# Performance work log

Measured on AMD Instinct MI355X. Metric: run time of the kernel, lower is better.

Reference implementation:

```python
import jax, jax.numpy as jnp
import numpy as np
from jax import lax

DIM = 512
HEADS = 8
HEAD_DIM = DIM // HEADS
FS = 56            # features_size -> H = W = 56
SR = 2             # sr_ratio
N = FS * FS        # query tokens = 3136
KN = (FS // SR) ** 2  # kv tokens = 784
B = 4
SCALE = HEAD_DIM ** -0.5
LN_EPS = 1e-5


def _relative_indices(fs):
    # matches generate_relative_distance: [[x, y] for x in range(fs) for y in range(fs)]
    coords = np.stack(np.meshgrid(np.arange(fs), np.arange(fs), indexing='ij'), -1).reshape(-1, 2)
    dist = coords[None, :, :] - coords[:, None, :] + (fs - 1)   # (N, N, 2), values in [0, 2fs-2]
    return jnp.asarray(dist, dtype=jnp.int32)


def setup_inputs() -> dict:
    key = jax.random.key(0)
    ks = jax.random.split(key, 8)
    s = 0.02
    return {
        'x':    jax.random.normal(ks[0], (B, DIM, FS, FS), jnp.float32),
        'Wq':   jax.random.normal(ks[1], (DIM, DIM), jnp.float32) * s,
        'Wkv':  jax.random.normal(ks[2], (DIM, 2 * DIM), jnp.float32) * s,
        'Wsr':  jax.random.normal(ks[3], (DIM, DIM, SR, SR), jnp.float32) * s,  # OIHW
        'b_sr': jnp.zeros((DIM,), jnp.float32),
        'gamma': jnp.ones((DIM,), jnp.float32),
        'beta':  jnp.zeros((DIM,), jnp.float32),
        'Wp':   jax.random.normal(ks[4], (DIM, DIM), jnp.float32) * s,
        'bp':   jnp.zeros((DIM,), jnp.float32),
        'pos':  jax.random.normal(ks[5], (2 * FS - 1, 2 * FS - 1), jnp.float32) * 0.2,
        'rel_idx': _relative_indices(FS),
    }


def reference(x, Wq, Wkv, Wsr, b_sr, gamma, beta, Wp, bp, pos, rel_idx):
    b, c, h, w = x.shape
    n = h * w
    xq = x.reshape(b, c, n).transpose(0, 2, 1)                      # B N C
    q = (xq @ Wq).reshape(b, n, HEADS, HEAD_DIM).transpose(0, 2, 1, 3)  # B h N d

    # spatial reduction of k/v: Conv2d(k=SR, s=SR) + LayerNorm
    xr = lax.conv_general_dilated(x, Wsr, (SR, SR), 'VALID',
                                  dimension_numbers=('NCHW', 'OIHW', 'NCHW'))
    xr = xr + b_sr[None, :, None, None]
    kn = xr.shape[2] * xr.shape[3]
    xkv = xr.reshape(b, c, kn).transpose(0, 2, 1)                   # B KN C
    mu = xkv.mean(-1, keepdims=True)
    var = ((xkv - mu) ** 2).mean(-1, keepdims=True)
    xkv = (xkv - mu) * lax.rsqrt(var + LN_EPS) * gamma + beta

    # kv projection; rearrange 'B N (dim h l) -> l B h N dim'
    kv = (xkv @ Wkv).reshape(b, kn, HEAD_DIM, HEADS, 2)
    k = kv[..., 0].transpose(0, 3, 1, 2)                            # B h KN d
    v = kv[..., 1].transpose(0, 3, 1, 2)                            # B h KN d

    attn = jnp.einsum('bhnd,bhmd->bhnm', q, k) * SCALE              # B h N KN
    bias = pos[rel_idx[:, :kn, 0], rel_idx[:, :kn, 1]]              # N KN gathered bias
    attn = jax.nn.softmax(attn + bias, axis=-1)

    out = jnp.einsum('bhnm,bhmd->bhnd', attn, v)                    # B h N d
    out = out.transpose(0, 2, 1, 3).reshape(b, n, c)                # B N C
    out = out @ Wp + bp
    return out.transpose(0, 2, 1).reshape(b, c, h, w)
```

## Files before the change

kernel.cpp:

```cpp
#include <hip/hip_runtime.h>
#include <hip/hip_bf16.h>
#include <cstdint>

constexpr int BATCH = 4;
constexpr int CDIM  = 512;
constexpr int NHEAD = 8;
constexpr int HD    = 64;
constexpr int FSP   = 56;
constexpr int NTOK  = FSP * FSP;
constexpr int KH    = 28;
constexpr int KNTOK = KH * KH;
constexpr float SCALE_ATT = 0.125f;
constexpr int BIAS_LD = 832;

typedef _Float16 f16;
typedef __attribute__((ext_vector_type(8))) _Float16 half8;
typedef __attribute__((ext_vector_type(4))) float  floatx4;

__global__ __launch_bounds__(256) void k_tsplit(const float* __restrict__ in,
                                                f16* __restrict__ oh,
                                                int R, int C,
                                                size_t inb, size_t outb) {
  __shared__ float t[64][65];
  const int tid = threadIdx.x;
  in += (size_t)blockIdx.z * inb;
  oh += (size_t)blockIdx.z * outb;
  const int r0 = blockIdx.x * 64, c0 = blockIdx.y * 64;
  const int rr = tid >> 2, cs = (tid & 3) * 16;
  const float* src = in + (size_t)(r0 + rr) * C + c0 + cs;
#pragma unroll
  for (int j = 0; j < 16; j += 4) *(float4*)&t[rr][cs + j] = *(const float4*)&src[j];
  __syncthreads();
  f16* dh = oh + (size_t)(c0 + rr) * R + r0 + cs;
#pragma unroll
  for (int j = 0; j < 16; ++j) dh[j] = (f16)t[cs + j][rr];
}

__global__ __launch_bounds__(256) void k_srprep(const float* __restrict__ Wsr,
                                                f16* __restrict__ oh) {
  const int o = blockIdx.x;
  const float* src = Wsr + (size_t)o * 2048;
  f16* dh = oh + (size_t)o * 2048;
  for (int kp = threadIdx.x; kp < 2048; kp += 256) {
    const int dd = kp >> 9, c = kp & 511;
    dh[kp] = (f16)src[c * 4 + dd];
  }
}

#define GSTR 40
struct GemmSmem { f16 A[128][GSTR]; f16 B[128][GSTR]; };

__device__ __forceinline__ void gemm_loop(GemmSmem* sm,
                                          const f16* __restrict__ aP,
                                          const f16* __restrict__ bP,
                                          int sr, int ss, int wm, int wn,
                                          int quad, int tx,
                                          floatx4 acc[4][4]) {
  half8 ra0 = *(const half8*)&aP[0];
  half8 ra1 = *(const half8*)&aP[8];
  half8 rb0 = *(const half8*)&bP[0];
  half8 rb1 = *(const half8*)&bP[8];
  for (int it = 0; it < 16; ++it) {
    *(half8*)&sm->A[sr][ss]     = ra0;
    *(half8*)&sm->A[sr][ss + 8] = ra1;
    *(half8*)&sm->B[sr][ss]     = rb0;
    *(half8*)&sm->B[sr][ss + 8] = rb1;
    __syncthreads();
    if (it + 1 < 16) {
      const f16* an = aP + (it + 1) * 32;
      const f16* bn = bP + (it + 1) * 32;
      ra0 = *(const half8*)&an[0]; ra1 = *(const half8*)&an[8];
      rb0 = *(const half8*)&bn[0]; rb1 = *(const half8*)&bn[8];
    }
    half8 ah[4];
#pragma unroll
    for (int i = 0; i < 4; ++i)
      ah[i] = *(const half8*)&sm->A[wm * 64 + i * 16 + tx][quad * 8];
#pragma unroll
    for (int j = 0; j < 4; ++j) {
      const half8 bh = *(const half8*)&sm->B[wn * 64 + j * 16 + tx][quad * 8];
#pragma unroll
      for (int i = 0; i < 4; ++i)
        acc[i][j] = __builtin_amdgcn_mfma_f32_16x16x32_f16(ah[i], bh, acc[i][j], 0, 0, 0);
    }
    __syncthreads();
  }
}

#define GEMM_PRE()                                                        \
  const int tid = threadIdx.x, lane = tid & 63, wv = tid >> 6;            \
  const int wm = wv & 1, wn = wv >> 1, quad = lane >> 4, tx = lane & 15;  \
  const int sr = tid >> 1, ss = (tid & 1) * 16;                           \
  floatx4 acc[4][4];                                                      \
  _Pragma("unroll") for (int i = 0; i < 4; ++i)                           \
  _Pragma("unroll") for (int j = 0; j < 4; ++j)                           \
      acc[i][j] = (floatx4){0.f, 0.f, 0.f, 0.f};

__global__ __launch_bounds__(256) void k_srconv(const f16* __restrict__ xT,
                                                const f16* __restrict__ WsrP,
                                                float* __restrict__ XRp) {
  __shared__ GemmSmem sm;
  const int m0 = blockIdx.x * 128, n0 = blockIdx.y * 128;
  const int b = blockIdx.z >> 2, kc = blockIdx.z & 3;
  GEMM_PRE();
  int am = m0 + sr; if (am >= KNTOK) am = 0;
  const int ii = am / KH, jj = am % KH;
  const int sp = 112 * ii + 2 * jj + (kc >> 1) * FSP + (kc & 1);
  const f16* aP = xT + (size_t)b * NTOK * CDIM + (size_t)sp * CDIM + ss;
  const f16* bP = WsrP + (size_t)(n0 + sr) * 2048 + kc * 512 + ss;
  gemm_loop(&sm, aP, bP, sr, ss, wm, wn, quad, tx, acc);
  float* dst = XRp + (size_t)(kc * BATCH + b) * KNTOK * CDIM;
#pragma unroll
  for (int i = 0; i < 4; ++i)
#pragma unroll
    for (int rg = 0; rg < 4; ++rg) {
      const int m = m0 + wm * 64 + i * 16 + quad * 4 + rg;
      if (m >= KNTOK) continue;
#pragma unroll
      for (int j = 0; j < 4; ++j)
        dst[(size_t)m * CDIM + n0 + wn * 64 + j * 16 + tx] = acc[i][j][rg];
    }
}

__global__ __launch_bounds__(256) void k_ln(const float* __restrict__ XRp,
                                            const float* __restrict__ b_sr,
                                            const float* __restrict__ gamma,
                                            const float* __restrict__ beta,
                                            f16* __restrict__ oh) {
  const int row = blockIdx.x;
  const size_t slab = (size_t)BATCH * KNTOK * CDIM;
  const float* p = XRp + (size_t)row * CDIM;
  const int tid = threadIdx.x;
  const float v0 = p[tid] + p[tid + slab] + p[tid + 2 * slab] + p[tid + 3 * slab]
                 + b_sr[tid];
  const float v1 = p[tid + 256] + p[tid + 256 + slab] + p[tid + 256 + 2 * slab]
                 + p[tid + 256 + 3 * slab] + b_sr[tid + 256];
  float s = v0 + v1;
  float s2 = v0 * v0 + v1 * v1;
#pragma unroll
  for (int mask = 32; mask >= 1; mask >>= 1) {
    s  += __shfl_xor(s, mask, 64);
    s2 += __shfl_xor(s2, mask, 64);
  }
  __shared__ float ws[4], ws2[4];
  const int wid = tid >> 6;
  if ((tid & 63) == 0) { ws[wid] = s; ws2[wid] = s2; }
  __syncthreads();
  const float ts  = ws[0] + ws[1] + ws[2] + ws[3];
  const float ts2 = ws2[0] + ws2[1] + ws2[2] + ws2[3];
  const float mu  = ts * (1.f / CDIM);
  const float var = ts2 * (1.f / CDIM) - mu * mu;
  const float rs  = rsqrtf(var + 1e-5f);
  const size_t base = (size_t)row * CDIM;
  oh[base + tid]       = (f16)((v0 - mu) * rs * gamma[tid] + beta[tid]);
  oh[base + tid + 256] = (f16)((v1 - mu) * rs * gamma[tid + 256] + beta[tid + 256]);
}

__global__ __launch_bounds__(256) void k_qkv(const f16* __restrict__ xT,
                                             const f16* __restrict__ WqT,
                                             f16* __restrict__ Qh,
                                             const f16* __restrict__ XRh,
                                             const f16* __restrict__ WkvT,
                                             f16* __restrict__ Kh,
                                             f16* __restrict__ Vt) {
  __shared__ GemmSmem sm;
  GEMM_PRE();
  int bid = blockIdx.x;
  if (bid < 400) {
    const int b = bid / 100, t = bid % 100;
    const int m0 = (t >> 2) * 128, n0 = (t & 3) * 128;
    int arow = m0 + sr; if (arow >= NTOK) arow = NTOK - 1;
    const f16* aP = xT + (size_t)b * NTOK * CDIM + (size_t)arow * CDIM + ss;
    const f16* bP = WqT + (size_t)(n0 + sr) * CDIM + ss;
    gemm_loop(&sm, aP, bP, sr, ss, wm, wn, quad, tx, acc);
    f16* qhB = Qh + (size_t)b * NTOK * CDIM;
#pragma unroll
    for (int i = 0; i < 4; ++i)
#pragma unroll
      for (int rg = 0; rg < 4; ++rg) {
        const int m = m0 + wm * 64 + i * 16 + quad * 4 + rg;
        if (m >= NTOK) continue;
#pragma unroll
        for (int j = 0; j < 4; ++j)
          qhB[(size_t)m * CDIM + n0 + wn * 64 + j * 16 + tx] = (f16)acc[i][j][rg];
      }
  } else {
    bid -= 400;
    const int b = bid / 56, w = bid % 56, nt = w / 7, mt = w % 7;
    const int m0 = mt * 128, n0 = nt * 128;
    int arow = m0 + sr; if (arow >= KNTOK) arow = KNTOK - 1;
    const f16* aP = XRh + (size_t)b * KNTOK * CDIM + (size_t)arow * CDIM + ss;
    const f16* bP = WkvT + (size_t)(n0 + sr) * CDIM + ss;
    gemm_loop(&sm, aP, bP, sr, ss, wm, wn, quad, tx, acc);
#pragma unroll
    for (int i = 0; i < 4; ++i)
#pragma unroll
      for (int rg = 0; rg < 4; ++rg) {
        const int m = m0 + wm * 64 + i * 16 + quad * 4 + rg;
        if (m >= KNTOK) continue;
#pragma unroll
        for (int j = 0; j < 4; ++j) {
          const int o2 = n0 + wn * 64 + j * 16 + tx;
          const int d = o2 >> 4, hh = (o2 >> 1) & 7;
          const float v = acc[i][j][rg];
          if (o2 & 1)
            Vt[((size_t)(b * NHEAD + hh) * HD + d) * KNTOK + m] = (f16)v;
          else
            Kh[((size_t)(b * NHEAD + hh) * KNTOK + m) * HD + d] = (f16)v;
        }
      }
  }
}

__global__ __launch_bounds__(256) void k_bias(const int* __restrict__ rel,
                                              const float* __restrict__ pos,
                                              float* __restrict__ biasT) {
  const int n = blockIdx.x;
  for (int i = threadIdx.x; i < BIAS_LD; i += 256) {
    const int jc = i >> 6, w = i & 63, txx = w >> 2, tt = w & 3;
    const int m = jc * 64 + tt * 16 + txx;
    float v = -30000.f;
    if (m < KNTOK) {
      const size_t o = ((size_t)n * NTOK + m) * 2;
      v = pos[rel[o] * 111 + rel[o + 1]];
    }
    biasT[(size_t)n * BIAS_LD + i] = v;
  }
}

#define LSTR 72
__global__ __launch_bounds__(256) void k_attn(const f16* __restrict__ Qh,
                                              const f16* __restrict__ Kh,
                                              const f16* __restrict__ Vt,
                                              const float* __restrict__ biasT,
                                              f16* __restrict__ Oh) {
  __shared__ f16 Qhs[64][LSTR], Khs[64][LSTR], Vts[64][LSTR];
  __shared__ f16 Ps[4][16][LSTR];
  const int b = blockIdx.x >> 3, h = blockIdx.x & 7;
  const int n0 = blockIdx.y * 64;
  const int tid = threadIdx.x, lane = tid & 63, wv = tid >> 6;
  const int quad = lane >> 4, tx = lane & 15;
  const int rr = tid >> 2, sg = (tid & 3) * 16;

  const f16* qhB = Qh + ((size_t)b * NTOK + n0) * CDIM + h * HD;
  const f16* khB = Kh + (size_t)(b * NHEAD + h) * KNTOK * HD;
  const f16* vtB = Vt + (size_t)(b * NHEAD + h) * HD * KNTOK;

  {
    const size_t off = (size_t)rr * CDIM + sg;
    *(half8*)&Qhs[rr][sg]     = *(const half8*)&qhB[off];
    *(half8*)&Qhs[rr][sg + 8] = *(const half8*)&qhB[off + 8];
  }

  size_t bbase_r[4];
#pragma unroll
  for (int r = 0; r < 4; ++r) {
    const int grow = n0 + wv * 16 + quad * 4 + r;
    bbase_r[r] = (size_t)grow * BIAS_LD + tx * 4;
  }

  floatx4 acc_o[4];
#pragma unroll
  for (int t = 0; t < 4; ++t) acc_o[t] = (floatx4){0.f, 0.f, 0.f, 0.f};
  float l_part[4] = {0.f, 0.f, 0.f, 0.f};
  __syncthreads();

  for (int jc = 0; jc < 13; ++jc) {
    const int mb = jc * 64;
    const half8 z = {0, 0, 0, 0, 0, 0, 0, 0};
    {
      const int m = mb + rr;
      if (m < KNTOK) {
        const size_t off = (size_t)m * HD + sg;
        *(half8*)&Khs[rr][sg]     = *(const half8*)&khB[off];
        *(half8*)&Khs[rr][sg + 8] = *(const half8*)&khB[off + 8];
      } else {
        *(half8*)&Khs[rr][sg] = z; *(half8*)&Khs[rr][sg + 8] = z;
      }
      if (mb + sg < KNTOK) {
        const size_t voff = (size_t)rr * KNTOK + mb + sg;
        *(half8*)&Vts[rr][sg]     = *(const half8*)&vtB[voff];
        *(half8*)&Vts[rr][sg + 8] = *(const half8*)&vtB[voff + 8];
      } else {
        *(half8*)&Vts[rr][sg] = z; *(half8*)&Vts[rr][sg + 8] = z;
      }
    }
    __syncthreads();

    floatx4 sc[4];
#pragma unroll
    for (int t = 0; t < 4; ++t) sc[t] = (floatx4){0.f, 0.f, 0.f, 0.f};
#pragma unroll
    for (int ks = 0; ks < 2; ++ks) {
      const int kk = ks * 32 + quad * 8;
      const half8 aqh = *(const half8*)&Qhs[wv * 16 + tx][kk];
#pragma unroll
      for (int t = 0; t < 4; ++t) {
        const half8 bkh = *(const half8*)&Khs[t * 16 + tx][kk];
        sc[t] = __builtin_amdgcn_mfma_f32_16x16x32_f16(aqh, bkh, sc[t], 0, 0, 0);
      }
    }

#pragma unroll
    for (int r = 0; r < 4; ++r) {
      const float4 bb = *(const float4*)&biasT[bbase_r[r] + jc * 64];
      const float p0 = __expf(fmaf(sc[0][r], SCALE_ATT, bb.x));
      const float p1 = __expf(fmaf(sc[1][r], SCALE_ATT, bb.y));
      const float p2 = __expf(fmaf(sc[2][r], SCALE_ATT, bb.z));
      const float p3 = __expf(fmaf(sc[3][r], SCALE_ATT, bb.w));
      l_part[r] += (p0 + p1) + (p2 + p3);
      const int prow = quad * 4 + r;
      Ps[wv][prow][0 * 16 + tx] = (f16)p0;
      Ps[wv][prow][1 * 16 + tx] = (f16)p1;
      Ps[wv][prow][2 * 16 + tx] = (f16)p2;
      Ps[wv][prow][3 * 16 + tx] = (f16)p3;
    }

#pragma unroll
    for (int ks = 0; ks < 2; ++ks) {
      const int kk = ks * 32 + quad * 8;
      const half8 ap = *(const half8*)&Ps[wv][tx][kk];
#pragma unroll
      for (int t = 0; t < 4; ++t) {
        const half8 bv = *(const half8*)&Vts[t * 16 + tx][kk];
        acc_o[t] = __builtin_amdgcn_mfma_f32_16x16x32_f16(ap, bv, acc_o[t], 0, 0, 0);
      }
    }
    __syncthreads();
  }

#pragma unroll
  for (int r = 0; r < 4; ++r) {
    float l = l_part[r];
#pragma unroll
    for (int msk = 1; msk < 16; msk <<= 1) l += __shfl_xor(l, msk, 64);
    const float inv = 1.f / l;
    const int grow = n0 + wv * 16 + quad * 4 + r;
    const size_t base = ((size_t)b * NTOK + grow) * CDIM + h * HD;
#pragma unroll
    for (int t = 0; t < 4; ++t)
      Oh[base + t * 16 + tx] = (f16)(acc_o[t][r] * inv);
  }
}

__global__ __launch_bounds__(256) void k_outproj(const f16* __restrict__ ah_,
                                                 const f16* __restrict__ wh,
                                                 const float* __restrict__ bp,
                                                 float* __restrict__ out) {
  __shared__ GemmSmem sm;
  const int b = blockIdx.z, m0 = blockIdx.x * 128, n0 = blockIdx.y * 128;
  GEMM_PRE();
  int arow = m0 + sr; if (arow >= NTOK) arow = NTOK - 1;
  const f16* aP = ah_ + (size_t)b * NTOK * CDIM + (size_t)arow * CDIM + ss;
  const f16* bP = wh + (size_t)(n0 + sr) * CDIM + ss;
  gemm_loop(&sm, aP, bP, sr, ss, wm, wn, quad, tx, acc);
#pragma unroll
  for (int j = 0; j < 4; ++j) {
    const int co = n0 + wn * 64 + j * 16 + tx;
    const float bpv = bp[co];
    float* obase = out + ((size_t)b * CDIM + co) * NTOK;
#pragma unroll
    for (int i = 0; i < 4; ++i) {
      const int mb4 = m0 + wm * 64 + i * 16 + quad * 4;
      if (mb4 < NTOK) {
        floatx4 v = acc[i][j] + bpv;
        *(floatx4*)&obase[mb4] = v;
      }
    }
  }
}

extern "C" void kernel_launch(void* const* d_in, const int* in_sizes, int n_in,
                              void* d_out, int out_size, void* d_ws, size_t ws_size,
                              hipStream_t stream) {
  const float* x     = (const float*)d_in[0];
  const float* Wq    = (const float*)d_in[1];
  const float* Wkv   = (const float*)d_in[2];
  const float* Wsr   = (const float*)d_in[3];
  const float* b_sr  = (const float*)d_in[4];
  const float* gamma = (const float*)d_in[5];
  const float* beta  = (const float*)d_in[6];
  const float* Wp    = (const float*)d_in[7];
  const float* bp    = (const float*)d_in[8];
  const float* pos   = (const float*)d_in[9];
  const int*   rel   = (const int*)d_in[10];
  float* out = (float*)d_out;

  char* p = (char*)d_ws;
  auto alloc = [&](size_t bytes) -> void* {
    void* r = (void*)p;
    p += (bytes + 255) & ~(size_t)255;
    return r;
  };
  const size_t SZ_BNC = (size_t)BATCH * NTOK * CDIM;
  const size_t SZ_BKC = (size_t)BATCH * KNTOK * CDIM;
  const size_t SZ_KV  = (size_t)BATCH * NHEAD * KNTOK * HD;

  f16* xT    = (f16*)alloc(SZ_BNC * 2);
  f16* WqT   = (f16*)alloc(512 * 512 * 2);
  f16* WkvT  = (f16*)alloc(1024 * 512 * 2);
  f16* WpT   = (f16*)alloc(512 * 512 * 2);
  f16* WsrP  = (f16*)alloc(512 * 2048 * 2);
  f16* Qh    = (f16*)alloc(SZ_BNC * 2);
  float* XRp = (float*)alloc(SZ_BKC * 4 * 4);
  f16* XRh   = (f16*)alloc(SZ_BKC * 2);
  f16* Vt    = (f16*)alloc(SZ_KV * 2);
  float* biasT = (float*)alloc((size_t)NTOK * BIAS_LD * 4);

  f16* Kh = (f16*)XRp;
  f16* Og = xT;

  const dim3 blk(256);
  k_tsplit<<<dim3(8, 49, BATCH), blk, 0, stream>>>(x, xT, CDIM, NTOK,
                                                   (size_t)CDIM * NTOK, (size_t)NTOK * CDIM);
  k_tsplit<<<dim3(8, 8, 1),  blk, 0, stream>>>(Wq,  WqT,  512, 512,  0, 0);
  k_tsplit<<<dim3(8, 16, 1), blk, 0, stream>>>(Wkv, WkvT, 512, 1024, 0, 0);
  k_tsplit<<<dim3(8, 8, 1),  blk, 0, stream>>>(Wp,  WpT,  512, 512,  0, 0);
  k_srprep<<<dim3(512),  blk, 0, stream>>>(Wsr, WsrP);
  k_bias  <<<dim3(NTOK), blk, 0, stream>>>(rel, pos, biasT);

  k_srconv<<<dim3(7, 4, BATCH * 4), blk, 0, stream>>>(xT, WsrP, XRp);
  k_ln    <<<dim3(BATCH * KNTOK),   blk, 0, stream>>>(XRp, b_sr, gamma, beta, XRh);
  k_qkv   <<<dim3(624),             blk, 0, stream>>>(xT, WqT, Qh, XRh, WkvT, Kh, Vt);
  k_attn  <<<dim3(BATCH * NHEAD, 49), blk, 0, stream>>>(Qh, Kh, Vt, biasT, Og);
  k_outproj<<<dim3(25, 4, BATCH),   blk, 0, stream>>>(Og, WpT, bp, out);
}
```

Baseline: 320.1 us.

## Merge prep kernels, use 64-row GEMM tiles, and prefetch K/V in attention

Folds all transpose, weight-repack and bias-gather kernels into one launch. All GEMMs move to 64x128 tiles, giving more blocks and no ragged M tiles for the 3136-row GEMMs. The Q projection now runs alongside the SR conv instead of alongside the KV projection. The attention loop prefetches the next K/V chunk into registers while computing the current one, using clamped indices instead of zero-fill. In exchange, half the threads sit idle during A-tile loads, and the clamped tail reads depend on the bias mask to stay correct.

```diff
diff --git a/kernel.cpp b/kernel.cpp
--- a/kernel.cpp
+++ b/kernel.cpp
@@ -17,109 +17,164 @@
 typedef __attribute__((ext_vector_type(8))) _Float16 half8;
 typedef __attribute__((ext_vector_type(4))) float  floatx4;
 
-__global__ __launch_bounds__(256) void k_tsplit(const float* __restrict__ in,
-                                                f16* __restrict__ oh,
-                                                int R, int C,
-                                                size_t inb, size_t outb) {
-  __shared__ float t[64][65];
-  const int tid = threadIdx.x;
-  in += (size_t)blockIdx.z * inb;
-  oh += (size_t)blockIdx.z * outb;
-  const int r0 = blockIdx.x * 64, c0 = blockIdx.y * 64;
+__device__ __forceinline__ void tr64(const float* __restrict__ in,
+                                     f16* __restrict__ out, int R, int C,
+                                     int r0, int c0, float (*sm)[65], int tid) {
   const int rr = tid >> 2, cs = (tid & 3) * 16;
   const float* src = in + (size_t)(r0 + rr) * C + c0 + cs;
 #pragma unroll
-  for (int j = 0; j < 16; j += 4) *(float4*)&t[rr][cs + j] = *(const float4*)&src[j];
+  for (int j = 0; j < 16; j += 4) *(float4*)&sm[rr][cs + j] = *(const float4*)&src[j];
   __syncthreads();
-  f16* dh = oh + (size_t)(c0 + rr) * R + r0 + cs;
-#pragma unroll
-  for (int j = 0; j < 16; ++j) dh[j] = (f16)t[cs + j][rr];
-}
-
-__global__ __launch_bounds__(256) void k_srprep(const float* __restrict__ Wsr,
-                                                f16* __restrict__ oh) {
-  const int o = blockIdx.x;
-  const float* src = Wsr + (size_t)o * 2048;
-  f16* dh = oh + (size_t)o * 2048;
-  for (int kp = threadIdx.x; kp < 2048; kp += 256) {
-    const int dd = kp >> 9, c = kp & 511;
-    dh[kp] = (f16)src[c * 4 + dd];
+  f16* dh = out + (size_t)(c0 + rr) * R + r0 + cs;
+#pragma unroll
+  for (int j = 0; j < 16; ++j) dh[j] = (f16)sm[cs + j][rr];
+}
+
+__global__ __launch_bounds__(256) void k_prep(const float* __restrict__ x,
+                                              const float* __restrict__ Wq,
+                                              const float* __restrict__ Wkv,
+                                              const float* __restrict__ Wp,
+                                              const float* __restrict__ Wsr,
+                                              const int* __restrict__ rel,
+                                              const float* __restrict__ pos,
+                                              f16* __restrict__ xT,
+                                              f16* __restrict__ WqT,
+                                              f16* __restrict__ WkvT,
+                                              f16* __restrict__ WpT,
+                                              f16* __restrict__ WsrP,
+                                              float* __restrict__ biasT) {
+  __shared__ float sm[64][65];
+  const int tid = threadIdx.x;
+  int bid = blockIdx.x;
+  if (bid < 1568) {
+    const int b = bid / 392, r = bid % 392;
+    tr64(x + (size_t)b * CDIM * NTOK, xT + (size_t)b * NTOK * CDIM,
+         CDIM, NTOK, (r % 8) * 64, (r / 8) * 64, sm, tid);
+    return;
+  }
+  bid -= 1568;
+  if (bid < 64)  { tr64(Wq,  WqT,  512, 512,  (bid % 8) * 64, (bid / 8) * 64, sm, tid); return; }
+  bid -= 64;
+  if (bid < 128) { tr64(Wkv, WkvT, 512, 1024, (bid % 8) * 64, (bid / 8) * 64, sm, tid); return; }
+  bid -= 128;
+  if (bid < 64)  { tr64(Wp,  WpT,  512, 512,  (bid % 8) * 64, (bid / 8) * 64, sm, tid); return; }
+  bid -= 64;
+  if (bid < 512) {
+    const float* src = Wsr + (size_t)bid * 2048;
+    f16* dh = WsrP + (size_t)bid * 2048;
+    for (int kp = tid; kp < 2048; kp += 256) {
+      const int dd = kp >> 9, c = kp & 511;
+      dh[kp] = (f16)src[c * 4 + dd];
+    }
+    return;
+  }
+  bid -= 512;
+  {
+    const int n = bid;
+    for (int i = tid; i < BIAS_LD; i += 256) {
+      const int jc = i >> 6, w = i & 63, txx = w >> 2, tt = w & 3;
+      const int m = jc * 64 + tt * 16 + txx;
+      float v = -30000.f;
+      if (m < KNTOK) {
+        const size_t o = ((size_t)n * NTOK + m) * 2;
+        v = pos[rel[o] * 111 + rel[o + 1]];
+      }
+      biasT[(size_t)n * BIAS_LD + i] = v;
+    }
   }
 }
 
 #define GSTR 40
-struct GemmSmem { f16 A[128][GSTR]; f16 B[128][GSTR]; };
-
-__device__ __forceinline__ void gemm_loop(GemmSmem* sm,
-                                          const f16* __restrict__ aP,
-                                          const f16* __restrict__ bP,
-                                          int sr, int ss, int wm, int wn,
-                                          int quad, int tx,
-                                          floatx4 acc[4][4]) {
-  half8 ra0 = *(const half8*)&aP[0];
-  half8 ra1 = *(const half8*)&aP[8];
-  half8 rb0 = *(const half8*)&bP[0];
-  half8 rb1 = *(const half8*)&bP[8];
+struct GemmSmem { f16 A[64][GSTR]; f16 B[128][GSTR]; };
+
+__device__ __forceinline__ void gemm_loop64(GemmSmem* sm,
+    const f16* __restrict__ aP, const f16* __restrict__ bP, bool doA,
+    int sr, int ss, int wm, int wn, int quad, int tx, floatx4 acc[2][4]) {
+  half8 ra0 = {0, 0, 0, 0, 0, 0, 0, 0}, ra1 = ra0;
+  if (doA) { ra0 = *(const half8*)&aP[0]; ra1 = *(const half8*)&aP[8]; }
+  half8 rb0 = *(const half8*)&bP[0], rb1 = *(const half8*)&bP[8];
   for (int it = 0; it < 16; ++it) {
-    *(half8*)&sm->A[sr][ss]     = ra0;
-    *(half8*)&sm->A[sr][ss + 8] = ra1;
-    *(half8*)&sm->B[sr][ss]     = rb0;
-    *(half8*)&sm->B[sr][ss + 8] = rb1;
+    if (doA) { *(half8*)&sm->A[sr][ss] = ra0; *(half8*)&sm->A[sr][ss + 8] = ra1; }
+    *(half8*)&sm->B[sr][ss] = rb0; *(half8*)&sm->B[sr][ss + 8] = rb1;
     __syncthreads();
     if (it + 1 < 16) {
       const f16* an = aP + (it + 1) * 32;
       const f16* bn = bP + (it + 1) * 32;
-      ra0 = *(const half8*)&an[0]; ra1 = *(const half8*)&an[8];
+      if (doA) { ra0 = *(const half8*)&an[0]; ra1 = *(const half8*)&an[8]; }
       rb0 = *(const half8*)&bn[0]; rb1 = *(const half8*)&bn[8];
     }
-    half8 ah[4];
-#pragma unroll
-    for (int i = 0; i < 4; ++i)
-      ah[i] = *(const half8*)&sm->A[wm * 64 + i * 16 + tx][quad * 8];
+    half8 ah[2];
+#pragma unroll
+    for (int i = 0; i < 2; ++i)
+      ah[i] = *(const half8*)&sm->A[wm * 32 + i * 16 + tx][quad * 8];
 #pragma unroll
     for (int j = 0; j < 4; ++j) {
       const half8 bh = *(const half8*)&sm->B[wn * 64 + j * 16 + tx][quad * 8];
 #pragma unroll
-      for (int i = 0; i < 4; ++i)
+      for (int i = 0; i < 2; ++i)
         acc[i][j] = __builtin_amdgcn_mfma_f32_16x16x32_f16(ah[i], bh, acc[i][j], 0, 0, 0);
     }
     __syncthreads();
   }
 }
 
-#define GEMM_PRE()                                                        \
+#define GEMM_PRE64()                                                      \
   const int tid = threadIdx.x, lane = tid & 63, wv = tid >> 6;            \
   const int wm = wv & 1, wn = wv >> 1, quad = lane >> 4, tx = lane & 15;  \
   const int sr = tid >> 1, ss = (tid & 1) * 16;                           \
-  floatx4 acc[4][4];                                                      \
-  _Pragma("unroll") for (int i = 0; i < 4; ++i)                           \
+  const bool doA = tid < 128;                                             \
+  floatx4 acc[2][4];                                                      \
+  _Pragma("unroll") for (int i = 0; i < 2; ++i)                           \
   _Pragma("unroll") for (int j = 0; j < 4; ++j)                           \
       acc[i][j] = (floatx4){0.f, 0.f, 0.f, 0.f};
 
-__global__ __launch_bounds__(256) void k_srconv(const f16* __restrict__ xT,
-                                                const f16* __restrict__ WsrP,
-                                                float* __restrict__ XRp) {
+__global__ __launch_bounds__(256) void k_gemmA(const f16* __restrict__ xT,
+                                               const f16* __restrict__ WqT,
+                                               f16* __restrict__ Qh,
+                                               const f16* __restrict__ WsrP,
+                                               float* __restrict__ XRp) {
   __shared__ GemmSmem sm;
-  const int m0 = blockIdx.x * 128, n0 = blockIdx.y * 128;
-  const int b = blockIdx.z >> 2, kc = blockIdx.z & 3;
-  GEMM_PRE();
-  int am = m0 + sr; if (am >= KNTOK) am = 0;
-  const int ii = am / KH, jj = am % KH;
-  const int sp = 112 * ii + 2 * jj + (kc >> 1) * FSP + (kc & 1);
-  const f16* aP = xT + (size_t)b * NTOK * CDIM + (size_t)sp * CDIM + ss;
-  const f16* bP = WsrP + (size_t)(n0 + sr) * 2048 + kc * 512 + ss;
-  gemm_loop(&sm, aP, bP, sr, ss, wm, wn, quad, tx, acc);
-  float* dst = XRp + (size_t)(kc * BATCH + b) * KNTOK * CDIM;
-#pragma unroll
-  for (int i = 0; i < 4; ++i)
-#pragma unroll
-    for (int rg = 0; rg < 4; ++rg) {
-      const int m = m0 + wm * 64 + i * 16 + quad * 4 + rg;
-      if (m >= KNTOK) continue;
-#pragma unroll
-      for (int j = 0; j < 4; ++j)
-        dst[(size_t)m * CDIM + n0 + wn * 64 + j * 16 + tx] = acc[i][j][rg];
-    }
+  GEMM_PRE64();
+  int bid = blockIdx.x;
+  if (bid < 784) {
+    const int b = bid / 196, r = bid % 196;
+    const int m0 = (r >> 2) * 64, n0 = (r & 3) * 128;
+    const f16* aP = xT + (size_t)b * NTOK * CDIM + (size_t)(m0 + sr) * CDIM + ss;
+    const f16* bP = WqT + (size_t)(n0 + sr) * CDIM + ss;
+    gemm_loop64(&sm, aP, bP, doA, sr, ss, wm, wn, quad, tx, acc);
+    f16* qhB = Qh + (size_t)b * NTOK * CDIM;
+#pragma unroll
+    for (int i = 0; i < 2; ++i)
+#pragma unroll
+      for (int rg = 0; rg < 4; ++rg) {
+        const int m = m0 + wm * 32 + i * 16 + quad * 4 + rg;
+#pragma unroll
+        for (int j = 0; j < 4; ++j)
+          qhB[(size_t)m * CDIM + n0 + wn * 64 + j * 16 + tx] = (f16)acc[i][j][rg];
+      }
+  } else {
+    bid -= 784;
+    const int bkc = bid / 52, r = bid % 52;
+    const int b = bkc >> 2, kc = bkc & 3;
+    const int m0 = (r >> 2) * 64, n0 = (r & 3) * 128;
+    int am = m0 + sr; if (am >= KNTOK) am = 0;
+    const int ii = am / KH, jj = am % KH;
+    const int sp = 112 * ii + 2 * jj + (kc >> 1) * FSP + (kc & 1);
+    const f16* aP = xT + (size_t)b * NTOK * CDIM + (size_t)sp * CDIM + ss;
+    const f16* bP = WsrP + (size_t)(n0 + sr) * 2048 + kc * 512 + ss;
+    gemm_loop64(&sm, aP, bP, doA, sr, ss, wm, wn, quad, tx, acc);
+    float* dst = XRp + (size_t)(kc * BATCH + b) * KNTOK * CDIM;
+#pragma unroll
+    for (int i = 0; i < 2; ++i)
+#pragma unroll
+      for (int rg = 0; rg < 4; ++rg) {
+        const int m = m0 + wm * 32 + i * 16 + quad * 4 + rg;
+        if (m >= KNTOK) continue;
+#pragma unroll
+        for (int j = 0; j < 4; ++j)
+          dst[(size_t)m * CDIM + n0 + wn * 64 + j * 16 + tx] = acc[i][j][rg];
+      }
+  }
 }
 
 __global__ __launch_bounds__(256) void k_ln(const float* __restrict__ XRp,
@@ -156,76 +211,36 @@
   oh[base + tid + 256] = (f16)((v1 - mu) * rs * gamma[tid + 256] + beta[tid + 256]);
 }
 
-__global__ __launch_bounds__(256) void k_qkv(const f16* __restrict__ xT,
-                                             const f16* __restrict__ WqT,
-                                             f16* __restrict__ Qh,
-                                             const f16* __restrict__ XRh,
-                                             const f16* __restrict__ WkvT,
-                                             f16* __restrict__ Kh,
-                                             f16* __restrict__ Vt) {
+__global__ __launch_bounds__(256) void k_kvproj(const f16* __restrict__ XRh,
+                                                const f16* __restrict__ WkvT,
+                                                f16* __restrict__ Kh,
+                                                f16* __restrict__ Vt) {
   __shared__ GemmSmem sm;
-  GEMM_PRE();
-  int bid = blockIdx.x;
-  if (bid < 400) {
-    const int b = bid / 100, t = bid % 100;
-    const int m0 = (t >> 2) * 128, n0 = (t & 3) * 128;
-    int arow = m0 + sr; if (arow >= NTOK) arow = NTOK - 1;
-    const f16* aP = xT + (size_t)b * NTOK * CDIM + (size_t)arow * CDIM + ss;
-    const f16* bP = WqT + (size_t)(n0 + sr) * CDIM + ss;
-    gemm_loop(&sm, aP, bP, sr, ss, wm, wn, quad, tx, acc);
-    f16* qhB = Qh + (size_t)b * NTOK * CDIM;
-#pragma unroll
-    for (int i = 0; i < 4; ++i)
-#pragma unroll
-      for (int rg = 0; rg < 4; ++rg) {
-        const int m = m0 + wm * 64 + i * 16 + quad * 4 + rg;
-        if (m >= NTOK) continue;
-#pragma unroll
-        for (int j = 0; j < 4; ++j)
-          qhB[(size_t)m * CDIM + n0 + wn * 64 + j * 16 + tx] = (f16)acc[i][j][rg];
-      }
-  } else {
-    bid -= 400;
-    const int b = bid / 56, w = bid % 56, nt = w / 7, mt = w % 7;
-    const int m0 = mt * 128, n0 = nt * 128;
-    int arow = m0 + sr; if (arow >= KNTOK) arow = KNTOK - 1;
-    const f16* aP = XRh + (size_t)b * KNTOK * CDIM + (size_t)arow * CDIM + ss;
-    const f16* bP = WkvT + (size_t)(n0 + sr) * CDIM + ss;
-    gemm_loop(&sm, aP, bP, sr, ss, wm, wn, quad, tx, acc);
-#pragma unroll
-    for (int i = 0; i < 4; ++i)
-#pragma unroll
-      for (int rg = 0; rg < 4; ++rg) {
-        const int m = m0 + wm * 64 + i * 16 + quad * 4 + rg;
-        if (m >= KNTOK) continue;
-#pragma unroll
-        for (int j = 0; j < 4; ++j) {
-          const int o2 = n0 + wn * 64 + j * 16 + tx;
-          const int d = o2 >> 4, hh = (o2 >> 1) & 7;
-          const float v = acc[i][j][rg];
-          if (o2 & 1)
-            Vt[((size_t)(b * NHEAD + hh) * HD + d) * KNTOK + m] = (f16)v;
-          else
-            Kh[((size_t)(b * NHEAD + hh) * KNTOK + m) * HD + d] = (f16)v;
-        }
-      }
-  }
-}
-
-__global__ __launch_bounds__(256) void k_bias(const int* __restrict__ rel,
-                                              const float* __restrict__ pos,
-                                              float* __restrict__ biasT) {
-  const int n = blockIdx.x;
-  for (int i = threadIdx.x; i < BIAS_LD; i += 256) {
-    const int jc = i >> 6, w = i & 63, txx = w >> 2, tt = w & 3;
-    const int m = jc * 64 + tt * 16 + txx;
-    float v = -30000.f;
-    if (m < KNTOK) {
-      const size_t o = ((size_t)n * NTOK + m) * 2;
-      v = pos[rel[o] * 111 + rel[o + 1]];
-    }
-    biasT[(size_t)n * BIAS_LD + i] = v;
-  }
+  GEMM_PRE64();
+  const int bid = blockIdx.x;
+  const int b = bid / 104, r = bid % 104;
+  const int m0 = (r >> 3) * 64, n0 = (r & 7) * 128;
+  int arow = m0 + sr; if (arow >= KNTOK) arow = KNTOK - 1;
+  const f16* aP = XRh + (size_t)b * KNTOK * CDIM + (size_t)arow * CDIM + ss;
+  const f16* bP = WkvT + (size_t)(n0 + sr) * CDIM + ss;
+  gemm_loop64(&sm, aP, bP, doA, sr, ss, wm, wn, quad, tx, acc);
+#pragma unroll
+  for (int i = 0; i < 2; ++i)
+#pragma unroll
+    for (int rg = 0; rg < 4; ++rg) {
+      const int m = m0 + wm * 32 + i * 16 + quad * 4 + rg;
+      if (m >= KNTOK) continue;
+#pragma unroll
+      for (int j = 0; j < 4; ++j) {
+        const int o2 = n0 + wn * 64 + j * 16 + tx;
+        const int d = o2 >> 4, hh = (o2 >> 1) & 7;
+        const float v = acc[i][j][rg];
+        if (o2 & 1)
+          Vt[((size_t)(b * NHEAD + hh) * HD + d) * KNTOK + m] = (f16)v;
+        else
+          Kh[((size_t)(b * NHEAD + hh) * KNTOK + m) * HD + d] = (f16)v;
+      }
+    }
 }
 
 #define LSTR 72
@@ -247,17 +262,21 @@
   const f16* vtB = Vt + (size_t)(b * NHEAD + h) * HD * KNTOK;
 
   {
-    const size_t off = (size_t)rr * CDIM + sg;
-    *(half8*)&Qhs[rr][sg]     = *(const half8*)&qhB[off];
-    *(half8*)&Qhs[rr][sg + 8] = *(const half8*)&qhB[off + 8];
+    const size_t qoff = (size_t)rr * CDIM + sg;
+    *(half8*)&Qhs[rr][sg]     = *(const half8*)&qhB[qoff];
+    *(half8*)&Qhs[rr][sg + 8] = *(const half8*)&qhB[qoff + 8];
+    const size_t koff = (size_t)rr * HD + sg;
+    *(half8*)&Khs[rr][sg]     = *(const half8*)&khB[koff];
+    *(half8*)&Khs[rr][sg + 8] = *(const half8*)&khB[koff + 8];
+    const size_t voff = (size_t)rr * KNTOK + sg;
+    *(half8*)&Vts[rr][sg]     = *(const half8*)&vtB[voff];
+    *(half8*)&Vts[rr][sg + 8] = *(const half8*)&vtB[voff + 8];
   }
 
   size_t bbase_r[4];
 #pragma unroll
-  for (int r = 0; r < 4; ++r) {
-    const int grow = n0 + wv * 16 + quad * 4 + r;
-    bbase_r[r] = (size_t)grow * BIAS_LD + tx * 4;
-  }
+  for (int r = 0; r < 4; ++r)
+    bbase_r[r] = (size_t)(n0 + wv * 16 + quad * 4 + r) * BIAS_LD + tx * 4;
 
   floatx4 acc_o[4];
 #pragma unroll
@@ -265,27 +284,19 @@
   float l_part[4] = {0.f, 0.f, 0.f, 0.f};
   __syncthreads();
 
+  half8 nk0, nk1, nv0, nv1;
   for (int jc = 0; jc < 13; ++jc) {
-    const int mb = jc * 64;
-    const half8 z = {0, 0, 0, 0, 0, 0, 0, 0};
-    {
-      const int m = mb + rr;
-      if (m < KNTOK) {
-        const size_t off = (size_t)m * HD + sg;
-        *(half8*)&Khs[rr][sg]     = *(const half8*)&khB[off];
-        *(half8*)&Khs[rr][sg + 8] = *(const half8*)&khB[off + 8];
-      } else {
-        *(half8*)&Khs[rr][sg] = z; *(half8*)&Khs[rr][sg + 8] = z;
-      }
-      if (mb + sg < KNTOK) {
-        const size_t voff = (size_t)rr * KNTOK + mb + sg;
-        *(half8*)&Vts[rr][sg]     = *(const half8*)&vtB[voff];
-        *(half8*)&Vts[rr][sg + 8] = *(const half8*)&vtB[voff + 8];
-      } else {
-        *(half8*)&Vts[rr][sg] = z; *(half8*)&Vts[rr][sg + 8] = z;
-      }
-    }
-    __syncthreads();
+    if (jc < 12) {
+      const int mbn = (jc + 1) * 64;
+      const int km = min(mbn + rr, KNTOK - 1);
+      const size_t koff = (size_t)km * HD + sg;
+      nk0 = *(const half8*)&khB[koff];
+      nk1 = *(const half8*)&khB[koff + 8];
+      const int vc = min(mbn + sg, KNTOK - 16);
+      const size_t voff = (size_t)rr * KNTOK + vc;
+      nv0 = *(const half8*)&vtB[voff];
+      nv1 = *(const half8*)&vtB[voff + 8];
+    }
 
     floatx4 sc[4];
 #pragma unroll
@@ -327,6 +338,13 @@
       }
     }
     __syncthreads();
+    if (jc < 12) {
+      *(half8*)&Khs[rr][sg]     = nk0;
+      *(half8*)&Khs[rr][sg + 8] = nk1;
+      *(half8*)&Vts[rr][sg]     = nv0;
+      *(half8*)&Vts[rr][sg + 8] = nv1;
+    }
+    __syncthreads();
   }
 
 #pragma unroll
@@ -343,29 +361,28 @@
   }
 }
 
-__global__ __launch_bounds__(256) void k_outproj(const f16* __restrict__ ah_,
-                                                 const f16* __restrict__ wh,
+__global__ __launch_bounds__(256) void k_outproj(const f16* __restrict__ Og,
+                                                 const f16* __restrict__ WpT,
                                                  const float* __restrict__ bp,
                                                  float* __restrict__ out) {
   __shared__ GemmSmem sm;
-  const int b = blockIdx.z, m0 = blockIdx.x * 128, n0 = blockIdx.y * 128;
-  GEMM_PRE();
-  int arow = m0 + sr; if (arow >= NTOK) arow = NTOK - 1;
-  const f16* aP = ah_ + (size_t)b * NTOK * CDIM + (size_t)arow * CDIM + ss;
-  const f16* bP = wh + (size_t)(n0 + sr) * CDIM + ss;
-  gemm_loop(&sm, aP, bP, sr, ss, wm, wn, quad, tx, acc);
+  GEMM_PRE64();
+  const int bid = blockIdx.x;
+  const int b = bid / 196, r = bid % 196;
+  const int m0 = (r >> 2) * 64, n0 = (r & 3) * 128;
+  const f16* aP = Og + (size_t)b * NTOK * CDIM + (size_t)(m0 + sr) * CDIM + ss;
+  const f16* bP = WpT + (size_t)(n0 + sr) * CDIM + ss;
+  gemm_loop64(&sm, aP, bP, doA, sr, ss, wm, wn, quad, tx, acc);
 #pragma unroll
   for (int j = 0; j < 4; ++j) {
     const int co = n0 + wn * 64 + j * 16 + tx;
     const float bpv = bp[co];
     float* obase = out + ((size_t)b * CDIM + co) * NTOK;
 #pragma unroll
-    for (int i = 0; i < 4; ++i) {
-      const int mb4 = m0 + wm * 64 + i * 16 + quad * 4;
-      if (mb4 < NTOK) {
-        floatx4 v = acc[i][j] + bpv;
-        *(floatx4*)&obase[mb4] = v;
-      }
+    for (int i = 0; i < 2; ++i) {
+      const int mb4 = m0 + wm * 32 + i * 16 + quad * 4;
+      floatx4 v = acc[i][j] + bpv;
+      *(floatx4*)&obase[mb4] = v;
     }
   }
 }
@@ -411,17 +428,11 @@
   f16* Og = xT;
 
   const dim3 blk(256);
-  k_tsplit<<<dim3(8, 49, BATCH), blk, 0, stream>>>(x, xT, CDIM, NTOK,
-                                                   (size_t)CDIM * NTOK, (size_t)NTOK * CDIM);
-  k_tsplit<<<dim3(8, 8, 1),  blk, 0, stream>>>(Wq,  WqT,  512, 512,  0, 0);
-  k_tsplit<<<dim3(8, 16, 1), blk, 0, stream>>>(Wkv, WkvT, 512, 1024, 0, 0);
-  k_tsplit<<<dim3(8, 8, 1),  blk, 0, stream>>>(Wp,  WpT,  512, 512,  0, 0);
-  k_srprep<<<dim3(512),  blk, 0, stream>>>(Wsr, WsrP);
-  k_bias  <<<dim3(NTOK), blk, 0, stream>>>(rel, pos, biasT);
-
-  k_srconv<<<dim3(7, 4, BATCH * 4), blk, 0, stream>>>(xT, WsrP, XRp);
-  k_ln    <<<dim3(BATCH * KNTOK),   blk, 0, stream>>>(XRp, b_sr, gamma, beta, XRh);
-  k_qkv   <<<dim3(624),             blk, 0, stream>>>(xT, WqT, Qh, XRh, WkvT, Kh, Vt);
-  k_attn  <<<dim3(BATCH * NHEAD, 49), blk, 0, stream>>>(Qh, Kh, Vt, biasT, Og);
-  k_outproj<<<dim3(25, 4, BATCH),   blk, 0, stream>>>(Og, WpT, bp, out);
-}
+  k_prep   <<<dim3(5472), blk, 0, stream>>>(x, Wq, Wkv, Wp, Wsr, rel, pos,
+                                            xT, WqT, WkvT, WpT, WsrP, biasT);
+  k_gemmA  <<<dim3(1616), blk, 0, stream>>>(xT, WqT, Qh, WsrP, XRp);
+  k_ln     <<<dim3(BATCH * KNTOK), blk, 0, stream>>>(XRp, b_sr, gamma, beta, XRh);
+  k_kvproj <<<dim3(416),  blk, 0, stream>>>(XRh, WkvT, Kh, Vt);
+  k_attn   <<<dim3(BATCH * NHEAD, 49), blk, 0, stream>>>(Qh, Kh, Vt, biasT, Og);
+  k_outproj<<<dim3(784),  blk, 0, stream>>>(Og, WpT, bp, out);
+}
```

New measurement: 305.4 us. 1.05x faster.
